# Kernel tuning notes

Hardware: AMD Instinct MI355X
Metric: run time of the kernel (lower is better)

## Reference

```python
import jax, jax.numpy as jnp
import numpy as np

C = 128   # d_pair, fixed by the fp8 tri-mul kernel assert
H = 128   # d_hidden


def layer_norm(x, w, b, eps=1e-5):
    m = jnp.mean(x, axis=-1, keepdims=True)
    v = jnp.mean(jnp.square(x - m), axis=-1, keepdims=True)
    return (x - m) * jax.lax.rsqrt(v + eps) * w + b


def setup_inputs() -> dict:
    key = jax.random.key(0)
    ks = jax.random.split(key, 12)
    B, N = 1, 512
    s_in = 1.0 / np.sqrt(C)
    s_h = 1.0 / np.sqrt(H)
    return {
        "z": jax.random.normal(ks[0], (B, N, N, C), jnp.float32),
        "mask": jnp.ones((B, N, N), jnp.float32),
        "ln_in_w": jnp.ones((C,), jnp.float32),
        "ln_in_b": jnp.zeros((C,), jnp.float32),
        "w_ap": jax.random.normal(ks[1], (C, H), jnp.float32) * s_in,
        "b_ap": jnp.zeros((H,), jnp.float32),
        "w_ag": jax.random.normal(ks[2], (C, H), jnp.float32) * s_in,
        "b_ag": jnp.zeros((H,), jnp.float32),
        "w_bp": jax.random.normal(ks[3], (C, H), jnp.float32) * s_in,
        "b_bp": jnp.zeros((H,), jnp.float32),
        "w_bg": jax.random.normal(ks[4], (C, H), jnp.float32) * s_in,
        "b_bg": jnp.zeros((H,), jnp.float32),
        "ln_out_w": jnp.ones((H,), jnp.float32),
        "ln_out_b": jnp.zeros((H,), jnp.float32),
        "w_o": jax.random.normal(ks[5], (H, C), jnp.float32) * s_h,
        "b_o": jnp.zeros((C,), jnp.float32),
        "w_g": jax.random.normal(ks[6], (C, C), jnp.float32) * s_in,
        "b_g": jnp.zeros((C,), jnp.float32),
    }


def reference(z, mask, ln_in_w, ln_in_b, w_ap, b_ap, w_ag, b_ag,
              w_bp, b_bp, w_bg, b_bg, ln_out_w, ln_out_b, w_o, b_o, w_g, b_g):
    # Triangular multiplicative update (outgoing), gated projections.
    z_ln = layer_norm(z, ln_in_w, ln_in_b)                      # [B,N,N,C]
    m = mask[..., None]                                         # [B,N,N,1]
    a = m * jax.nn.sigmoid(z_ln @ w_ag + b_ag) * (z_ln @ w_ap + b_ap)
    b = m * jax.nn.sigmoid(z_ln @ w_bg + b_bg) * (z_ln @ w_bp + b_bp)
    # outgoing: x[b,i,j,c] = sum_k a[b,i,k,c] * b[b,j,k,c]
    x = jnp.einsum("bikc,bjkc->bijc", a, b)                     # [B,N,N,H]
    x = layer_norm(x, ln_out_w, ln_out_b)
    g = jax.nn.sigmoid(z_ln @ w_g + b_g)                        # output gate
    return g * (x @ w_o + b_o)
```

## Files before the change

kernel.cpp:

```cpp
#include <hip/hip_runtime.h>
#include <hip/hip_bf16.h>
#include <stdint.h>

#define NDIM 512
#define NN (NDIM*NDIM)
#define CDIM 128
#define LDSP 136

typedef __attribute__((ext_vector_type(8))) short short8;
typedef __attribute__((ext_vector_type(4))) short short4v;
typedef __attribute__((ext_vector_type(4))) float f32x4;
typedef __attribute__((ext_vector_type(8))) _Float16 half8;
typedef unsigned long long ull;

__device__ __forceinline__ unsigned short f2h(float f) {
    union { _Float16 h; unsigned short u; } v;
    v.h = (_Float16)f;
    return v.u;
}
__device__ __forceinline__ float h2f(unsigned short u) {
    union { _Float16 h; unsigned short u; } v;
    v.u = u;
    return (float)v.h;
}
__device__ __forceinline__ f32x4 mfma16(short8 a, short8 b, f32x4 c) {
    return __builtin_amdgcn_mfma_f32_16x16x32_f16(
        __builtin_bit_cast(half8, a), __builtin_bit_cast(half8, b), c, 0, 0, 0);
}
__device__ __forceinline__ void gl_lds16(const void* g, void* l) {
    __builtin_amdgcn_global_load_lds((const __attribute__((address_space(1))) void*)g,
                                     (__attribute__((address_space(3))) void*)l,
                                     16, 0, 0);
}

__global__ void k0_prep(const float* __restrict__ w_ag, const float* __restrict__ w_ap,
                        const float* __restrict__ w_bg, const float* __restrict__ w_bp,
                        const float* __restrict__ w_g,  const float* __restrict__ w_o,
                        unsigned short* __restrict__ Wfrag, unsigned short* __restrict__ Wo_t)
{
    int idx = blockIdx.x * 256 + threadIdx.x;
    if (idx < 10240) {
        int lane = idx & 63;
        int n  = (idx >> 6) & 3;
        int kk = (idx >> 8) & 3;
        int h  = (idx >> 10) & 1;
        int s  = idx >> 11;
        const float* w = (s==0) ? w_ag : (s==1) ? w_ap : (s==2) ? w_bg : (s==3) ? w_bp : w_g;
        int col = h*64 + n*16 + (lane & 15);
        int k0  = kk*32 + (lane >> 4)*8;
        short8 pk;
        #pragma unroll
        for (int e = 0; e < 8; e++)
            pk[e] = (short)f2h(w[(k0 + e)*128 + col]);
        *(short8*)(Wfrag + (size_t)idx*8) = pk;
    } else if (idx < 10240 + 16384) {
        int i2 = idx - 10240;
        int cc = i2 >> 7, hh = i2 & 127;
        Wo_t[i2] = f2h(w_o[hh*128 + cc]);
    }
}

__global__ __launch_bounds__(512, 2) void k1_proj(
    const float* __restrict__ z, const float* __restrict__ mask,
    const float* __restrict__ lnw, const float* __restrict__ lnb,
    const unsigned short* __restrict__ Wfrag,
    const float* __restrict__ b_ag, const float* __restrict__ b_ap,
    const float* __restrict__ b_bg, const float* __restrict__ b_bp,
    unsigned short* __restrict__ a_t, unsigned short* __restrict__ b_t,
    unsigned short* __restrict__ zln)
{
    __shared__ unsigned short zb[64*LDSP];
    __shared__ float mask_s[64];
    __shared__ float lnw_s[128];
    __shared__ float lnb_s[128];
    __shared__ float bias_s[512];

    const int t = threadIdx.x;
    const int pos0 = blockIdx.x * 64;
    const int wave = t >> 6, lane = t & 63;
    const int wl = wave & 1;
    const int hh = (wave >> 1) & 1;
    const int pr = wave >> 2;
    const int lr = lane & 15, lh = lane >> 4;

    if (t < 128) {
        lnw_s[t] = lnw[t];
        lnb_s[t] = lnb[t];
    }
    if (t < 64) mask_s[t] = mask[pos0 + t];
    {
        int s = t >> 7, c = t & 127;
        const float* bp = (s==0) ? b_ag : (s==1) ? b_ap : (s==2) ? b_bg : b_bp;
        bias_s[t] = bp[c];
    }

    float v[32];
    float s0 = 0.f, s1 = 0.f;
    const int row4 = t >> 2, q = t & 3;
    if (t < 256) {
        const float* zr = z + (size_t)(pos0 + row4) * CDIM + q * 32;
        #pragma unroll
        for (int i = 0; i < 8; i++) {
            float4 qv = *(const float4*)(zr + i*4);
            v[i*4+0] = qv.x; v[i*4+1] = qv.y; v[i*4+2] = qv.z; v[i*4+3] = qv.w;
        }
        #pragma unroll
        for (int i = 0; i < 32; i++) { s0 += v[i]; s1 += v[i]*v[i]; }
        s0 += __shfl_xor(s0, 1);
        s1 += __shfl_xor(s1, 1);
        s0 += __shfl_xor(s0, 2);
        s1 += __shfl_xor(s1, 2);
    }
    __syncthreads();
    if (t < 256) {
        float m  = s0 * (1.f/128.f);
        float va = s1 * (1.f/128.f) - m*m;
        float rs = rsqrtf(va + 1e-5f);
        unsigned short* zo = zln + (size_t)(pos0 + row4)*CDIM + q*32;
        #pragma unroll
        for (int i = 0; i < 4; i++) {
            short8 pk;
            #pragma unroll
            for (int j = 0; j < 8; j++) {
                int c = q*32 + i*8 + j;
                pk[j] = (short)f2h((v[i*8+j]-m)*rs*lnw_s[c] + lnb_s[c]);
            }
            *(short8*)&zb[row4*LDSP + q*32 + i*8] = pk;
            *(short8*)(zo + i*8) = pk;
        }
    }
    __syncthreads();

    const int rowA0 = (wl*32 + lr)*LDSP;
    const int rowA1 = (wl*32 + 16 + lr)*LDSP;
    const unsigned short* wfl = Wfrag + (size_t)lane*8;

    auto gemmh = [&](int s, int h, f32x4 (&acc)[2][4]) {
        const unsigned short* wf = wfl + (size_t)(s*2 + h)*8192;
        #pragma unroll
        for (int m = 0; m < 2; m++)
            #pragma unroll
            for (int n = 0; n < 4; n++) { f32x4 zz = {0.f,0.f,0.f,0.f}; acc[m][n] = zz; }
        #pragma unroll
        for (int st = 0; st < 2; st++) {
            short8 wbuf[8];
            #pragma unroll
            for (int i = 0; i < 8; i++)
                wbuf[i] = *(const short8*)(wf + (st*8 + i)*512);
            #pragma unroll
            for (int k2 = 0; k2 < 2; k2++) {
                const int kk = st*2 + k2;
                const int k0 = kk*32 + lh*8;
                short8 af0 = *(const short8*)&zb[rowA0 + k0];
                short8 af1 = *(const short8*)&zb[rowA1 + k0];
                #pragma unroll
                for (int n = 0; n < 4; n++) {
                    acc[0][n] = mfma16(af0, wbuf[k2*4 + n], acc[0][n]);
                    acc[1][n] = mfma16(af1, wbuf[k2*4 + n], acc[1][n]);
                }
            }
        }
    };

    auto pair_half = [&](int sG, int sP, int h, unsigned short* dstg) {
        f32x4 G[2][4], P[2][4];
        gemmh(sG, h, G);
        gemmh(sP, h, P);
        const int odd = lh & 1;
        const int base = wl*32 + lh*4 + (odd ? 12 : 0);
        #pragma unroll
        for (int n = 0; n < 4; n++) {
            int col = h*64 + n*16 + lr;
            float bgv = bias_s[sG*128 + col];
            float bpv = bias_s[sP*128 + col];
            union { short4v v; ull u; } p0, p1;
            #pragma unroll
            for (int r = 0; r < 4; r++) {
                float g0 = 1.f / (1.f + __expf(-(G[0][n][r] + bgv)));
                p0.v[r] = (short)f2h(mask_s[wl*32 + lh*4 + r] * g0 * (P[0][n][r] + bpv));
                float g1 = 1.f / (1.f + __expf(-(G[1][n][r] + bgv)));
                p1.v[r] = (short)f2h(mask_s[wl*32 + 16 + lh*4 + r] * g1 * (P[1][n][r] + bpv));
            }
            ull r0 = __shfl_xor(p0.u, 16);
            ull r1 = __shfl_xor(p1.u, 16);
            union { ull u[2]; short8 v; } outv;
            outv.u[0] = odd ? r1 : p0.u;
            outv.u[1] = odd ? p1.u : r0;
            *(short8*)(dstg + (size_t)col*NN + pos0 + base) = outv.v;
        }
    };

    if (pr == 0) pair_half(0, 1, hh, a_t);
    else         pair_half(2, 3, hh, b_t);
}

#define K2_SMEM 34816
__global__ __launch_bounds__(256, 2) void k2_einsum(
    const unsigned short* __restrict__ a_t,
    const unsigned short* __restrict__ b_t,
    unsigned short* __restrict__ x_t)
{
    __shared__ char smem[K2_SMEM];

    const int c  = blockIdx.y;
    const int ti = (blockIdx.x >> 2) * 128;
    const int tj = (blockIdx.x & 3) * 128;
    const int t = threadIdx.x;
    const int wave = t >> 6, lane = t & 63;
    const int lr = lane & 15, lh = lane >> 4;
    const int wm = wave >> 1, wn = wave & 1;

    unsigned short* As = (unsigned short*)smem;
    unsigned short* Bs = (unsigned short*)(smem + 16384);

    const unsigned short* Ag = a_t + (size_t)c*NN + (size_t)ti*NDIM;
    const unsigned short* Bg = b_t + (size_t)c*NN + (size_t)tj*NDIM;

    const int srow = wave*32 + (lane >> 3);
    const int scol = ((lane & 7)*8) ^ ((lane >> 3) << 3);
    const int rsw  = (lr & 7) << 3;

    f32x4 acc[4][4] = {};

    for (int k0 = 0; k0 < NDIM; k0 += 64) {
        __syncthreads();
        #pragma unroll
        for (int it = 0; it < 4; it++) {
            int r = srow + it*8;
            gl_lds16(Ag + (size_t)r*NDIM + k0 + scol, (void*)(As + (wave*32 + it*8)*64));
            gl_lds16(Bg + (size_t)r*NDIM + k0 + scol, (void*)(Bs + (wave*32 + it*8)*64));
        }
        asm volatile("s_waitcnt vmcnt(0)" ::: "memory");
        __syncthreads();
        #pragma unroll
        for (int kk = 0; kk < 2; kk++) {
            const int kof = (kk*32 + lh*8) ^ rsw;
            short8 af[4], bfr[4];
            #pragma unroll
            for (int m = 0; m < 4; m++)
                af[m] = *(const short8*)&As[(wm*64 + m*16 + lr)*64 + kof];
            #pragma unroll
            for (int n = 0; n < 4; n++)
                bfr[n] = *(const short8*)&Bs[(wn*64 + n*16 + lr)*64 + kof];
            #pragma unroll
            for (int m = 0; m < 4; m++)
                #pragma unroll
                for (int n = 0; n < 4; n++)
                    acc[m][n] = mfma16(af[m], bfr[n], acc[m][n]);
        }
    }
    __syncthreads();

    unsigned short* eb = (unsigned short*)smem;
    #pragma unroll
    for (int m = 0; m < 4; m++) {
        int row = wm*64 + m*16 + lh*4;
        #pragma unroll
        for (int n = 0; n < 4; n++) {
            int col = wn*64 + n*16 + lr;
            #pragma unroll
            for (int r = 0; r < 4; r++)
                eb[(row + r)*136 + col] = f2h(acc[m][n][r]);
        }
    }
    __syncthreads();
    {
        const int row = t >> 1, half = t & 1;
        unsigned short* dst = x_t + (size_t)c*NN + (size_t)(ti + row)*NDIM + tj + half*64;
        #pragma unroll
        for (int i = 0; i < 8; i++)
            *(short8*)(dst + i*8) = *(const short8*)(eb + row*136 + half*64 + i*8);
    }
}

__global__ __launch_bounds__(256, 2) void k3_out(
    const unsigned short* __restrict__ x_t,
    const unsigned short* __restrict__ zln,
    const unsigned short* __restrict__ Wfrag,
    const unsigned short* __restrict__ Wo_t,
    const float* __restrict__ lnw, const float* __restrict__ lnb,
    const float* __restrict__ b_o, const float* __restrict__ b_g,
    float* __restrict__ out)
{
    __shared__ unsigned short xb[128*LDSP];
    __shared__ unsigned short zl[128*LDSP];
    __shared__ float lnw_s[128];
    __shared__ float lnb_s[128];
    __shared__ float bo_s[128];
    __shared__ float bg_s[128];

    const int t = threadIdx.x;
    const int pos0 = blockIdx.x * 128;
    const int tid2 = t >> 1, half = t & 1;
    const int wave = t >> 6, lane = t & 63;
    const int lr = lane & 15, lh = lane >> 4;

    if (t < 128) {
        lnw_s[t] = lnw[t]; lnb_s[t] = lnb[t];
        bo_s[t] = b_o[t];  bg_s[t] = b_g[t];
    }

    {
        const unsigned short* src = x_t + (size_t)tid2*NN + pos0 + half*64;
        unsigned short* dst = xb + tid2*LDSP + half*64;
        #pragma unroll
        for (int i = 0; i < 8; i++)
            *(short8*)(dst + i*8) = *(const short8*)(src + i*8);
    }
    __syncthreads();

    {
        float v[64];
        float s0 = 0.f, s1 = 0.f;
        #pragma unroll
        for (int i = 0; i < 64; i++) {
            float x = h2f(xb[(half*64 + i)*LDSP + tid2]);
            v[i] = x; s0 += x; s1 += x*x;
        }
        s0 += __shfl_xor(s0, 1);
        s1 += __shfl_xor(s1, 1);
        float m  = s0 * (1.f/128.f);
        float va = s1 * (1.f/128.f) - m*m;
        float rs = rsqrtf(va + 1e-5f);
        #pragma unroll
        for (int i = 0; i < 64; i++) {
            int cc = half*64 + i;
            zl[tid2*LDSP + cc] = f2h((v[i]-m)*rs*lnw_s[cc] + lnb_s[cc]);
        }
    }
    __syncthreads();

    {
        const unsigned short* src = Wo_t + ((size_t)tid2*128 + half*64);
        unsigned short* dst = xb + tid2*LDSP + half*64;
        #pragma unroll
        for (int i = 0; i < 8; i++)
            *(short8*)(dst + i*8) = *(const short8*)(src + i*8);
    }
    __syncthreads();

    const int rowA0 = (wave*32 + lr)*LDSP;
    const int rowA1 = (wave*32 + 16 + lr)*LDSP;

    f32x4 acc1[2][8];
    #pragma unroll
    for (int m = 0; m < 2; m++)
        #pragma unroll
        for (int n = 0; n < 8; n++) { f32x4 zz = {0.f,0.f,0.f,0.f}; acc1[m][n] = zz; }
    #pragma unroll
    for (int kk = 0; kk < 4; kk++) {
        const int k0 = kk*32 + lh*8;
        short8 af0 = *(const short8*)&zl[rowA0 + k0];
        short8 af1 = *(const short8*)&zl[rowA1 + k0];
        #pragma unroll
        for (int n = 0; n < 8; n++) {
            short8 bf = *(const short8*)&xb[(n*16 + lr)*LDSP + k0];
            acc1[0][n] = mfma16(af0, bf, acc1[0][n]);
            acc1[1][n] = mfma16(af1, bf, acc1[1][n]);
        }
    }
    __syncthreads();

    {
        const unsigned short* src = zln + (size_t)(pos0 + tid2)*CDIM + half*64;
        unsigned short* dst = zl + tid2*LDSP + half*64;
        #pragma unroll
        for (int i = 0; i < 8; i++)
            *(short8*)(dst + i*8) = *(const short8*)(src + i*8);
    }
    __syncthreads();

    f32x4 acc2[2][8];
    #pragma unroll
    for (int m = 0; m < 2; m++)
        #pragma unroll
        for (int n = 0; n < 8; n++) { f32x4 zz = {0.f,0.f,0.f,0.f}; acc2[m][n] = zz; }
    const unsigned short* wfl = Wfrag + (size_t)lane*8;
    #pragma unroll
    for (int h = 0; h < 2; h++) {
        const unsigned short* wf = wfl + (size_t)(8 + h)*8192;
        #pragma unroll
        for (int st = 0; st < 2; st++) {
            short8 wbuf[8];
            #pragma unroll
            for (int i = 0; i < 8; i++)
                wbuf[i] = *(const short8*)(wf + (st*8 + i)*512);
            #pragma unroll
            for (int k2 = 0; k2 < 2; k2++) {
                const int kk = st*2 + k2;
                const int k0 = kk*32 + lh*8;
                short8 af0 = *(const short8*)&zl[rowA0 + k0];
                short8 af1 = *(const short8*)&zl[rowA1 + k0];
                #pragma unroll
                for (int n = 0; n < 4; n++) {
                    acc2[0][h*4+n] = mfma16(af0, wbuf[k2*4 + n], acc2[0][h*4+n]);
                    acc2[1][h*4+n] = mfma16(af1, wbuf[k2*4 + n], acc2[1][h*4+n]);
                }
            }
        }
    }

    #pragma unroll
    for (int m = 0; m < 2; m++) {
        int rb = wave*32 + m*16 + lh*4;
        #pragma unroll
        for (int n = 0; n < 8; n++) {
            int col = n*16 + lr;
            float bo = bo_s[col];
            float bg = bg_s[col];
            #pragma unroll
            for (int r = 0; r < 4; r++) {
                float gv = 1.f / (1.f + __expf(-(acc2[m][n][r] + bg)));
                out[(size_t)(pos0 + rb + r)*CDIM + col] = gv * (acc1[m][n][r] + bo);
            }
        }
    }
}

extern "C" void kernel_launch(void* const* d_in, const int* in_sizes, int n_in,
                              void* d_out, int out_size, void* d_ws, size_t ws_size,
                              hipStream_t stream) {
    const float* z        = (const float*)d_in[0];
    const float* mask     = (const float*)d_in[1];
    const float* ln_in_w  = (const float*)d_in[2];
    const float* ln_in_b  = (const float*)d_in[3];
    const float* w_ap     = (const float*)d_in[4];
    const float* b_ap     = (const float*)d_in[5];
    const float* w_ag     = (const float*)d_in[6];
    const float* b_ag     = (const float*)d_in[7];
    const float* w_bp     = (const float*)d_in[8];
    const float* b_bp     = (const float*)d_in[9];
    const float* w_bg     = (const float*)d_in[10];
    const float* b_bg     = (const float*)d_in[11];
    const float* ln_out_w = (const float*)d_in[12];
    const float* ln_out_b = (const float*)d_in[13];
    const float* w_o      = (const float*)d_in[14];
    const float* b_o      = (const float*)d_in[15];
    const float* w_g      = (const float*)d_in[16];
    const float* b_g      = (const float*)d_in[17];

    char* ws = (char*)d_ws;
    const size_t BUF = (size_t)NN * 128 * 2;
    unsigned short* a_t   = (unsigned short*)(ws);
    unsigned short* b_t   = (unsigned short*)(ws + BUF);
    unsigned short* zln   = (unsigned short*)(ws + 2*BUF);
    unsigned short* x_t   = (unsigned short*)(ws + 3*BUF);
    unsigned short* Wfrag = (unsigned short*)(ws + 4*BUF);
    unsigned short* Wo_t  = (unsigned short*)(ws + 4*BUF + (size_t)10240*8*2);

    k0_prep<<<104, 256, 0, stream>>>(w_ag, w_ap, w_bg, w_bp, w_g, w_o, Wfrag, Wo_t);
    k1_proj<<<NN/64, 512, 0, stream>>>(z, mask, ln_in_w, ln_in_b, Wfrag,
                                       b_ag, b_ap, b_bg, b_bp, a_t, b_t, zln);
    k2_einsum<<<dim3(16, 128), 256, 0, stream>>>(a_t, b_t, x_t);
    k3_out<<<NN/128, 256, 0, stream>>>(x_t, zln, Wfrag, Wo_t, ln_out_w, ln_out_b,
                                       b_o, b_g, (float*)d_out);
}
```

Before: 303.4 us.

## Split input layernorm from projection kernel and keep weights in registers

Splits the fused LN+projection kernel in two. The first kernel normalises z and writes the fp16 zln buffer. The second reads zln straight from global memory with no LDS staging, holds the full G and P weight fragments in registers, and loops over two row halves per wave so each weight load is reused. The goal is to drop the LDS and barrier cost and raise occupancy in the projection. In exchange it adds an extra kernel launch and a global round trip of zln, which is written anyway for k3.

```diff
diff --git a/kernel.cpp b/kernel.cpp
--- a/kernel.cpp
+++ b/kernel.cpp
@@ -60,126 +60,127 @@
     }
 }
 
-__global__ __launch_bounds__(512, 2) void k1_proj(
-    const float* __restrict__ z, const float* __restrict__ mask,
+__global__ __launch_bounds__(256, 8) void k1a_ln(
+    const float* __restrict__ z,
     const float* __restrict__ lnw, const float* __restrict__ lnb,
+    unsigned short* __restrict__ zln)
+{
+    __shared__ float lnw_s[128];
+    __shared__ float lnb_s[128];
+    const int t = threadIdx.x;
+    if (t < 128) { lnw_s[t] = lnw[t]; lnb_s[t] = lnb[t]; }
+    const int tid2 = t >> 1, half = t & 1;
+    const int pos = blockIdx.x * 128 + tid2;
+
+    float v[64];
+    float s0 = 0.f, s1 = 0.f;
+    {
+        const float* zr = z + (size_t)pos * CDIM + half * 64;
+        #pragma unroll
+        for (int i = 0; i < 16; i++) {
+            float4 q = *(const float4*)(zr + i*4);
+            v[i*4+0] = q.x; v[i*4+1] = q.y; v[i*4+2] = q.z; v[i*4+3] = q.w;
+        }
+        #pragma unroll
+        for (int i = 0; i < 64; i++) { s0 += v[i]; s1 += v[i]*v[i]; }
+        s0 += __shfl_xor(s0, 1);
+        s1 += __shfl_xor(s1, 1);
+    }
+    __syncthreads();
+    {
+        float m  = s0 * (1.f/128.f);
+        float va = s1 * (1.f/128.f) - m*m;
+        float rs = rsqrtf(va + 1e-5f);
+        unsigned short* zo = zln + (size_t)pos*CDIM + half*64;
+        #pragma unroll
+        for (int i = 0; i < 8; i++) {
+            short8 pk;
+            #pragma unroll
+            for (int j = 0; j < 8; j++) {
+                int c = half*64 + i*8 + j;
+                pk[j] = (short)f2h((v[i*8+j]-m)*rs*lnw_s[c] + lnb_s[c]);
+            }
+            *(short8*)(zo + i*8) = pk;
+        }
+    }
+}
+
+__global__ __launch_bounds__(256, 3) void k1b_proj(
+    const unsigned short* __restrict__ zln,
+    const float* __restrict__ mask,
     const unsigned short* __restrict__ Wfrag,
     const float* __restrict__ b_ag, const float* __restrict__ b_ap,
     const float* __restrict__ b_bg, const float* __restrict__ b_bp,
-    unsigned short* __restrict__ a_t, unsigned short* __restrict__ b_t,
-    unsigned short* __restrict__ zln)
+    unsigned short* __restrict__ a_t, unsigned short* __restrict__ b_t)
 {
-    __shared__ unsigned short zb[64*LDSP];
-    __shared__ float mask_s[64];
-    __shared__ float lnw_s[128];
-    __shared__ float lnb_s[128];
-    __shared__ float bias_s[512];
-
     const int t = threadIdx.x;
     const int pos0 = blockIdx.x * 64;
     const int wave = t >> 6, lane = t & 63;
-    const int wl = wave & 1;
-    const int hh = (wave >> 1) & 1;
-    const int pr = wave >> 2;
+    const int hh = wave & 1;
+    const int pr = wave >> 1;
     const int lr = lane & 15, lh = lane >> 4;
-
-    if (t < 128) {
-        lnw_s[t] = lnw[t];
-        lnb_s[t] = lnb[t];
-    }
-    if (t < 64) mask_s[t] = mask[pos0 + t];
-    {
-        int s = t >> 7, c = t & 127;
-        const float* bp = (s==0) ? b_ag : (s==1) ? b_ap : (s==2) ? b_bg : b_bp;
-        bias_s[t] = bp[c];
-    }
-
-    float v[32];
-    float s0 = 0.f, s1 = 0.f;
-    const int row4 = t >> 2, q = t & 3;
-    if (t < 256) {
-        const float* zr = z + (size_t)(pos0 + row4) * CDIM + q * 32;
-        #pragma unroll
-        for (int i = 0; i < 8; i++) {
-            float4 qv = *(const float4*)(zr + i*4);
-            v[i*4+0] = qv.x; v[i*4+1] = qv.y; v[i*4+2] = qv.z; v[i*4+3] = qv.w;
-        }
-        #pragma unroll
-        for (int i = 0; i < 32; i++) { s0 += v[i]; s1 += v[i]*v[i]; }
-        s0 += __shfl_xor(s0, 1);
-        s1 += __shfl_xor(s1, 1);
-        s0 += __shfl_xor(s0, 2);
-        s1 += __shfl_xor(s1, 2);
-    }
-    __syncthreads();
-    if (t < 256) {
-        float m  = s0 * (1.f/128.f);
-        float va = s1 * (1.f/128.f) - m*m;
-        float rs = rsqrtf(va + 1e-5f);
-        unsigned short* zo = zln + (size_t)(pos0 + row4)*CDIM + q*32;
-        #pragma unroll
-        for (int i = 0; i < 4; i++) {
-            short8 pk;
-            #pragma unroll
-            for (int j = 0; j < 8; j++) {
-                int c = q*32 + i*8 + j;
-                pk[j] = (short)f2h((v[i*8+j]-m)*rs*lnw_s[c] + lnb_s[c]);
-            }
-            *(short8*)&zb[row4*LDSP + q*32 + i*8] = pk;
-            *(short8*)(zo + i*8) = pk;
-        }
-    }
-    __syncthreads();
-
-    const int rowA0 = (wl*32 + lr)*LDSP;
-    const int rowA1 = (wl*32 + 16 + lr)*LDSP;
+    const int sG = pr*2, sP = pr*2 + 1;
+
+    unsigned short* dstg = pr ? b_t : a_t;
+    const float* bgp = pr ? b_bg : b_ag;
+    const float* bpp = pr ? b_bp : b_ap;
+
     const unsigned short* wfl = Wfrag + (size_t)lane*8;
-
-    auto gemmh = [&](int s, int h, f32x4 (&acc)[2][4]) {
-        const unsigned short* wf = wfl + (size_t)(s*2 + h)*8192;
+    const unsigned short* wfG = wfl + (size_t)(sG*2 + hh)*8192;
+    const unsigned short* wfP = wfl + (size_t)(sP*2 + hh)*8192;
+    short8 wG[16], wP[16];
+    #pragma unroll
+    for (int i = 0; i < 16; i++) {
+        wG[i] = *(const short8*)(wfG + i*512);
+        wP[i] = *(const short8*)(wfP + i*512);
+    }
+
+    const int odd = lh & 1;
+
+    #pragma unroll
+    for (int wl = 0; wl < 2; wl++) {
+        const unsigned short* zbase = zln + (size_t)(pos0 + wl*32)*CDIM;
+        f32x4 G[2][4], P[2][4];
         #pragma unroll
         for (int m = 0; m < 2; m++)
             #pragma unroll
-            for (int n = 0; n < 4; n++) { f32x4 zz = {0.f,0.f,0.f,0.f}; acc[m][n] = zz; }
-        #pragma unroll
-        for (int st = 0; st < 2; st++) {
-            short8 wbuf[8];
-            #pragma unroll
-            for (int i = 0; i < 8; i++)
-                wbuf[i] = *(const short8*)(wf + (st*8 + i)*512);
-            #pragma unroll
-            for (int k2 = 0; k2 < 2; k2++) {
-                const int kk = st*2 + k2;
-                const int k0 = kk*32 + lh*8;
-                short8 af0 = *(const short8*)&zb[rowA0 + k0];
-                short8 af1 = *(const short8*)&zb[rowA1 + k0];
-                #pragma unroll
-                for (int n = 0; n < 4; n++) {
-                    acc[0][n] = mfma16(af0, wbuf[k2*4 + n], acc[0][n]);
-                    acc[1][n] = mfma16(af1, wbuf[k2*4 + n], acc[1][n]);
-                }
-            }
-        }
-    };
-
-    auto pair_half = [&](int sG, int sP, int h, unsigned short* dstg) {
-        f32x4 G[2][4], P[2][4];
-        gemmh(sG, h, G);
-        gemmh(sP, h, P);
-        const int odd = lh & 1;
+            for (int n = 0; n < 4; n++) {
+                f32x4 zz = {0.f,0.f,0.f,0.f};
+                G[m][n] = zz; P[m][n] = zz;
+            }
+        #pragma unroll
+        for (int kk = 0; kk < 4; kk++) {
+            const int k0 = kk*32 + lh*8;
+            short8 af0 = *(const short8*)(zbase + (size_t)lr*CDIM + k0);
+            short8 af1 = *(const short8*)(zbase + (size_t)(16 + lr)*CDIM + k0);
+            #pragma unroll
+            for (int n = 0; n < 4; n++) {
+                G[0][n] = mfma16(af0, wG[kk*4 + n], G[0][n]);
+                G[1][n] = mfma16(af1, wG[kk*4 + n], G[1][n]);
+                P[0][n] = mfma16(af0, wP[kk*4 + n], P[0][n]);
+                P[1][n] = mfma16(af1, wP[kk*4 + n], P[1][n]);
+            }
+        }
+
         const int base = wl*32 + lh*4 + (odd ? 12 : 0);
+        float m0[4], m1[4];
+        #pragma unroll
+        for (int r = 0; r < 4; r++) {
+            m0[r] = mask[pos0 + wl*32 + lh*4 + r];
+            m1[r] = mask[pos0 + wl*32 + 16 + lh*4 + r];
+        }
         #pragma unroll
         for (int n = 0; n < 4; n++) {
-            int col = h*64 + n*16 + lr;
-            float bgv = bias_s[sG*128 + col];
-            float bpv = bias_s[sP*128 + col];
+            int col = hh*64 + n*16 + lr;
+            float bgv = bgp[col];
+            float bpv = bpp[col];
             union { short4v v; ull u; } p0, p1;
             #pragma unroll
             for (int r = 0; r < 4; r++) {
                 float g0 = 1.f / (1.f + __expf(-(G[0][n][r] + bgv)));
-                p0.v[r] = (short)f2h(mask_s[wl*32 + lh*4 + r] * g0 * (P[0][n][r] + bpv));
+                p0.v[r] = (short)f2h(m0[r] * g0 * (P[0][n][r] + bpv));
                 float g1 = 1.f / (1.f + __expf(-(G[1][n][r] + bgv)));
-                p1.v[r] = (short)f2h(mask_s[wl*32 + 16 + lh*4 + r] * g1 * (P[1][n][r] + bpv));
+                p1.v[r] = (short)f2h(m1[r] * g1 * (P[1][n][r] + bpv));
             }
             ull r0 = __shfl_xor(p0.u, 16);
             ull r1 = __shfl_xor(p1.u, 16);
@@ -188,10 +189,7 @@
             outv.u[1] = odd ? p1.u : r0;
             *(short8*)(dstg + (size_t)col*NN + pos0 + base) = outv.v;
         }
-    };
-
-    if (pr == 0) pair_half(0, 1, hh, a_t);
-    else         pair_half(2, 3, hh, b_t);
+    }
 }
 
 #define K2_SMEM 34816
@@ -449,8 +447,9 @@
     unsigned short* Wo_t  = (unsigned short*)(ws + 4*BUF + (size_t)10240*8*2);
 
     k0_prep<<<104, 256, 0, stream>>>(w_ag, w_ap, w_bg, w_bp, w_g, w_o, Wfrag, Wo_t);
-    k1_proj<<<NN/64, 512, 0, stream>>>(z, mask, ln_in_w, ln_in_b, Wfrag,
-                                       b_ag, b_ap, b_bg, b_bp, a_t, b_t, zln);
+    k1a_ln<<<NN/128, 256, 0, stream>>>(z, ln_in_w, ln_in_b, zln);
+    k1b_proj<<<NN/64, 256, 0, stream>>>(zln, mask, Wfrag,
+                                        b_ag, b_ap, b_bg, b_bp, a_t, b_t);
     k2_einsum<<<dim3(16, 128), 256, 0, stream>>>(a_t, b_t, x_t);
     k3_out<<<NN/128, 256, 0, stream>>>(x_t, zln, Wfrag, Wo_t, ln_out_w, ln_out_b,
                                        b_o, b_g, (float*)d_out);
```

Result: slower. 518.5 us (+70.9%).
